# Performance work log

Hardware: AMD Instinct MI355X
Metric: run time of the kernel (lower is better)

## Reference

```python
import jax, jax.numpy as jnp
import numpy as np

DIM = 1024
NUM_HEADS = 16
HEAD_DIM = 64
SCALE = 1.0 / np.sqrt(float(HEAD_DIM))


def setup_inputs() -> dict:
    key = jax.random.key(0)
    ks = jax.random.split(key, 11)
    B, S, D = 2, 4096, DIM
    glorot = lambda k, shape: jax.random.uniform(
        k, shape, jnp.float32,
        -jnp.sqrt(6.0 / (shape[0] + shape[1])), jnp.sqrt(6.0 / (shape[0] + shape[1])))
    return {
        "x": jax.random.normal(ks[0], (B, S, D), jnp.float32),
        "Wq": glorot(ks[1], (D, NUM_HEADS * HEAD_DIM)),
        "bq": jnp.zeros((NUM_HEADS * HEAD_DIM,), jnp.float32),
        "Wk": glorot(ks[2], (D, NUM_HEADS * HEAD_DIM)),
        "bk": jnp.zeros((NUM_HEADS * HEAD_DIM,), jnp.float32),
        "Wv": glorot(ks[3], (D, NUM_HEADS * HEAD_DIM)),
        "bv": jnp.zeros((NUM_HEADS * HEAD_DIM,), jnp.float32),
        "Wqt": glorot(ks[4], (D, D)),
        "bqt": jnp.zeros((D,), jnp.float32),
        "Wo": glorot(ks[5], (D, D)),
        "bo": jnp.zeros((D,), jnp.float32),
        "num_anchor_tokens": 512,
    }


def _split_heads(t):
    # [B, T, H*Dh] -> [B, H, T, Dh]
    B, T, _ = t.shape
    return t.reshape(B, T, NUM_HEADS, HEAD_DIM).transpose(0, 2, 1, 3)


def reference(x, Wq, bq, Wk, bk, Wv, bv, Wqt, bqt, Wo, bo, num_anchor_tokens):
    B, S, D = x.shape
    A = num_anchor_tokens  # static Python int
    anchors = x[:, :A, :]            # [B, A, D]
    queries = x[:, A:, :]            # [B, S-A, D]

    anchor_q = _split_heads(anchors @ Wq + bq)   # [B, H, A, Dh]
    anchor_k = _split_heads(anchors @ Wk + bk)   # [B, H, A, Dh]
    anchor_v = _split_heads(anchors @ Wv + bv)   # [B, H, A, Dh]
    query_q = _split_heads(queries @ Wqt + bqt)  # [B, H, S-A, Dh]

    combined_q = jnp.concatenate([anchor_q, query_q], axis=2)  # [B, H, S, Dh]
    scores = jnp.einsum("bhsd,bhad->bhsa", combined_q, anchor_k) * SCALE
    attn = jax.nn.softmax(scores, axis=-1)        # [B, H, S, A]
    out = jnp.einsum("bhsa,bhad->bhsd", attn, anchor_v)  # [B, H, S, Dh]
    out = out.transpose(0, 2, 1, 3).reshape(B, S, D)
    return out @ Wo + bo
```

## Files before the change

### kernel.cpp

```cpp
#include <hip/hip_runtime.h>
#include <hip/hip_bf16.h>
#include <math.h>
#include <stdint.h>

typedef _Float16 f16;
typedef _Float16 f16x8 __attribute__((ext_vector_type(8)));
typedef _Float16 f16x4 __attribute__((ext_vector_type(4)));
typedef float f32x4 __attribute__((ext_vector_type(4)));

#define DIM   1024
#define NH    16
#define HD    64
#define BB    2
#define SS    4096
#define AA    512
#define SCALE 0.125f
#define EXP_C1 0.18033688011112043f
#define EXP_C2 (-2.8853900817779268f)

#define GLOAD_LDS16(g, l)                                                                   \
  __builtin_amdgcn_global_load_lds((const __attribute__((address_space(1))) uint32_t*)(g),  \
                                   (__attribute__((address_space(3))) uint32_t*)(l), 16, 0, 0)

static const size_t OFF_XH  = 0;
static const size_t OFF_WT  = 8388608;
static const size_t OFF_QC  = OFF_WT + 5u*1048576u;
static const size_t OFF_KB  = OFF_QC + 8388608u;
static const size_t OFF_VT  = OFF_KB + 1048576u;
static const size_t OFF_AO  = OFF_VT + 1048576u;

__global__ __launch_bounds__(256) void cast_x_kernel(const float* __restrict__ x,
                                                     f16* __restrict__ xh) {
    size_t i = ((size_t)blockIdx.x * 256 + threadIdx.x) * 4;
    float4 v = *reinterpret_cast<const float4*>(x + i);
    f16x4 o;
    o[0] = (f16)v.x; o[1] = (f16)v.y; o[2] = (f16)v.z; o[3] = (f16)v.w;
    *reinterpret_cast<f16x4*>(xh + i) = o;
}

__global__ __launch_bounds__(256) void wcast_kernel(const float* W0, const float* W1,
                                                    const float* W2, const float* W3,
                                                    const float* W4,
                                                    f16* T0, f16* T1, f16* T2, f16* T3, f16* T4) {
    __shared__ float tile[32][33];
    const float* W; f16* T;
    switch (blockIdx.z) {
        case 0: W = W0; T = T0; break;
        case 1: W = W1; T = T1; break;
        case 2: W = W2; T = T2; break;
        case 3: W = W3; T = T3; break;
        default: W = W4; T = T4; break;
    }
    int tx = threadIdx.x, ty = threadIdx.y;
    int gx = blockIdx.x * 32, gy = blockIdx.y * 32;
#pragma unroll
    for (int i = 0; i < 32; i += 8)
        tile[ty + i][tx] = W[(size_t)(gy + ty + i) * DIM + gx + tx];
    __syncthreads();
#pragma unroll
    for (int i = 0; i < 32; i += 8)
        T[(size_t)(gx + ty + i) * DIM + gy + tx] = (f16)tile[tx][ty + i];
}

struct GemmOut {
    const f16* Bt;
    const float* bias;
    int mode;
    void* out;
    int sdim;
    int soff;
};

__global__ __launch_bounds__(256) void gemm_kernel(const f16* __restrict__ A,
                                                   int rows_per_b, int a_row_off,
                                                   GemmOut o0, GemmOut o1, GemmOut o2) {
    __shared__ __align__(16) f16 As[128 * 32];
    __shared__ __align__(16) f16 Bs[128 * 32];

    GemmOut o = (blockIdx.z == 0) ? o0 : ((blockIdx.z == 1) ? o1 : o2);

    const int t    = threadIdx.x;
    const int wid  = t >> 6;
    const int lane = t & 63;
    const int lr   = lane & 15;
    const int lg   = lane >> 4;
    const int br   = blockIdx.x, bc = blockIdx.y;

    const int b      = (br * 128) / rows_per_b;
    const int s_base = (br * 128) % rows_per_b;

    const int srow = (wid << 4) + (lane >> 2);
    const int sch  = ((lane & 3) ^ ((lane >> 3) & 3)) << 3;
    const f16* Ap = A + ((size_t)b * SS + a_row_off + s_base + srow) * DIM + sch;
    const f16* Bp = o.Bt + ((size_t)(bc * 128 + srow)) * DIM + sch;
    f16* AsB = As + (wid << 9);
    f16* BsB = Bs + (wid << 9);

    const int wr = (wid >> 1) * 64;
    const int wc = (wid & 1) * 64;

    f32x4 acc[4][4] = {};

    for (int k0 = 0; k0 < DIM; k0 += 32) {
        GLOAD_LDS16(Ap + k0, AsB);
        GLOAD_LDS16(Ap + k0 + (size_t)64 * DIM, AsB + 2048);
        GLOAD_LDS16(Bp + k0, BsB);
        GLOAD_LDS16(Bp + k0 + (size_t)64 * DIM, BsB + 2048);
        __syncthreads();

        f16x8 af[4], bf[4];
#pragma unroll
        for (int m = 0; m < 4; m++) {
            const int r = wr + m * 16 + lr;
            af[m] = *reinterpret_cast<const f16x8*>(&As[r * 32 + ((lg ^ ((r >> 1) & 3)) << 3)]);
        }
#pragma unroll
        for (int n = 0; n < 4; n++) {
            const int r = wc + n * 16 + lr;
            bf[n] = *reinterpret_cast<const f16x8*>(&Bs[r * 32 + ((lg ^ ((r >> 1) & 3)) << 3)]);
        }
#pragma unroll
        for (int m = 0; m < 4; m++)
#pragma unroll
            for (int n = 0; n < 4; n++)
                acc[m][n] = __builtin_amdgcn_mfma_f32_16x16x32_f16(af[m], bf[n], acc[m][n], 0, 0, 0);
        __syncthreads();
    }

#pragma unroll
    for (int m = 0; m < 4; m++) {
        const int row_local = wr + m * 16 + lg * 4;
#pragma unroll
        for (int n = 0; n < 4; n++) {
            const int c  = bc * 128 + wc + n * 16 + lr;
            const float bv = o.bias[c];
            const int h = c >> 6, d = c & 63;
#pragma unroll
            for (int q = 0; q < 4; q++) {
                const int s_local = s_base + row_local + q;
                const float val = acc[m][n][q] + bv;
                if (o.mode == 2) {
                    ((float*)o.out)[((size_t)b * SS + o.soff + s_local) * DIM + c] = val;
                } else if (o.mode == 0) {
                    const int out_s = o.soff + s_local;
                    ((f16*)o.out)[(((size_t)(b * NH + h)) * o.sdim + out_s) * HD + d] = (f16)val;
                } else {
                    ((f16*)o.out)[(((size_t)(b * NH + h)) * HD + d) * AA + (o.soff + s_local)] = (f16)val;
                }
            }
        }
    }
}

__global__ __launch_bounds__(256) void attn_kernel(const f16* __restrict__ qc,
                                                   const f16* __restrict__ kb,
                                                   const f16* __restrict__ vt,
                                                   f16* __restrict__ ao) {
    __shared__ __align__(16) f16 Ks[2][64 * 64];
    __shared__ __align__(16) f16 Vs[2][64 * 64];
    __shared__ __align__(16) f16 Ps[4][16][64];

    const int t    = threadIdx.x;
    const int wid  = t >> 6;
    const int lane = t & 63;
    const int lr   = lane & 15;
    const int lg   = lane >> 4;
    const int qt   = blockIdx.x;
    const int h    = blockIdx.y;
    const int b    = blockIdx.z;
    const size_t bh = (size_t)b * NH + h;

    const int qrow = qt * 64 + wid * 16 + lr;
    const f16* qp = qc + (bh * SS + qrow) * HD + lg * 8;
    const f16x8 qa0 = *reinterpret_cast<const f16x8*>(qp);
    const f16x8 qa1 = *reinterpret_cast<const f16x8*>(qp + 32);

    const int sr_k = wid * 16 + (lane >> 3);
    const f16* kg = kb + bh * (size_t)AA * HD;
    const f16* vg = vt + bh * (size_t)HD * AA;

    f32x4 acc[4] = {};
    float rsum[4] = {0.f, 0.f, 0.f, 0.f};

#define ATTN_STAGE(buf, a0)                                                          \
    {                                                                                \
        _Pragma("unroll")                                                            \
        for (int i = 0; i < 2; i++) {                                                \
            const int r  = sr_k + i * 8;                                             \
            const int ck = (((lane & 7) ^ (r & 7)) << 3);                            \
            GLOAD_LDS16(kg + (size_t)((a0) + r) * HD + ck,                           \
                        &Ks[buf][(wid * 16 + i * 8) * 64]);                          \
            GLOAD_LDS16(vg + (size_t)r * AA + (a0) + ck,                             \
                        &Vs[buf][(wid * 16 + i * 8) * 64]);                          \
        }                                                                            \
    }

    ATTN_STAGE(0, 0);
    asm volatile("s_waitcnt vmcnt(0)");
    __syncthreads();

    int cur = 0;
    for (int at = 0; at < AA / 64; ++at) {
        if (at < AA / 64 - 1) ATTN_STAGE(cur ^ 1, (at + 1) * 64);

        f32x4 s[4];
#pragma unroll
        for (int n = 0; n < 4; n++) {
            const int r = n * 16 + lr;
            const int x = r & 7;
            f16x8 kf0 = *reinterpret_cast<const f16x8*>(&Ks[cur][r * 64 + ((lg ^ x) << 3)]);
            f16x8 kf1 = *reinterpret_cast<const f16x8*>(&Ks[cur][r * 64 + (((lg + 4) ^ x) << 3)]);
            f32x4 z = {};
            z = __builtin_amdgcn_mfma_f32_16x16x32_f16(qa0, kf0, z, 0, 0, 0);
            z = __builtin_amdgcn_mfma_f32_16x16x32_f16(qa1, kf1, z, 0, 0, 0);
            s[n] = z;
        }

#pragma unroll
        for (int n = 0; n < 4; n++) {
#pragma unroll
            for (int q = 0; q < 4; q++) {
                const float p = exp2f(fmaf(s[n][q], EXP_C1, EXP_C2));
                rsum[q] += p;
                const int row = lg * 4 + q;
                Ps[wid][row][(((2 * n + (lr >> 3)) ^ (row & 7)) << 3) + (lr & 7)] = (f16)p;
            }
        }
        const f16x8 pa0 = *reinterpret_cast<const f16x8*>(&Ps[wid][lr][(lg ^ (lr & 7)) << 3]);
        const f16x8 pa1 = *reinterpret_cast<const f16x8*>(&Ps[wid][lr][((lg + 4) ^ (lr & 7)) << 3]);

#pragma unroll
        for (int n = 0; n < 4; n++) {
            const int d = n * 16 + lr;
            const int x = d & 7;
            f16x8 vf0 = *reinterpret_cast<const f16x8*>(&Vs[cur][d * 64 + ((lg ^ x) << 3)]);
            f16x8 vf1 = *reinterpret_cast<const f16x8*>(&Vs[cur][d * 64 + (((lg + 4) ^ x) << 3)]);
            acc[n] = __builtin_amdgcn_mfma_f32_16x16x32_f16(pa0, vf0, acc[n], 0, 0, 0);
            acc[n] = __builtin_amdgcn_mfma_f32_16x16x32_f16(pa1, vf1, acc[n], 0, 0, 0);
        }

        asm volatile("s_waitcnt vmcnt(0)");
        __syncthreads();
        cur ^= 1;
    }

#pragma unroll
    for (int off = 1; off < 16; off <<= 1) {
#pragma unroll
        for (int q = 0; q < 4; q++) rsum[q] += __shfl_xor(rsum[q], off);
    }
#pragma unroll
    for (int q = 0; q < 4; q++) {
        const float inv = 1.0f / rsum[q];
        const int row = qt * 64 + wid * 16 + lg * 4 + q;
#pragma unroll
        for (int n = 0; n < 4; n++) {
            ao[((size_t)b * SS + row) * DIM + h * HD + n * 16 + lr] = (f16)(acc[n][q] * inv);
        }
    }
}

extern "C" void kernel_launch(void* const* d_in, const int* in_sizes, int n_in,
                              void* d_out, int out_size, void* d_ws, size_t ws_size,
                              hipStream_t stream) {
    const float* x   = (const float*)d_in[0];
    const float* Wq  = (const float*)d_in[1];
    const float* bq  = (const float*)d_in[2];
    const float* Wk  = (const float*)d_in[3];
    const float* bk  = (const float*)d_in[4];
    const float* Wv  = (const float*)d_in[5];
    const float* bv  = (const float*)d_in[6];
    const float* Wqt = (const float*)d_in[7];
    const float* bqt = (const float*)d_in[8];
    const float* Wo  = (const float*)d_in[9];
    const float* bo  = (const float*)d_in[10];

    f16* ws   = (f16*)d_ws;
    f16* xh   = ws + OFF_XH;
    f16* wtq  = ws + OFF_WT;
    f16* wtk  = wtq + 1048576u;
    f16* wtv  = wtk + 1048576u;
    f16* wtqt = wtv + 1048576u;
    f16* wto  = wtqt + 1048576u;
    f16* qc   = ws + OFF_QC;
    f16* kbuf = ws + OFF_KB;
    f16* vtb  = ws + OFF_VT;
    f16* ao   = ws + OFF_AO;

    cast_x_kernel<<<8192, 256, 0, stream>>>(x, xh);
    wcast_kernel<<<dim3(32, 32, 5), dim3(32, 8), 0, stream>>>(Wq, Wk, Wv, Wqt, Wo,
                                                              wtq, wtk, wtv, wtqt, wto);

    GemmOut oq { wtq, bq, 0, qc,   SS, 0 };
    GemmOut ok { wtk, bk, 0, kbuf, AA, 0 };
    GemmOut ov { wtv, bv, 1, vtb,  AA, 0 };
    gemm_kernel<<<dim3(8, 8, 3), 256, 0, stream>>>(xh, 512, 0, oq, ok, ov);

    GemmOut oqt { wtqt, bqt, 0, qc, SS, 512 };
    gemm_kernel<<<dim3(56, 8, 1), 256, 0, stream>>>(xh, 3584, 512, oqt, oqt, oqt);

    attn_kernel<<<dim3(64, NH, BB), 256, 0, stream>>>(qc, kbuf, vtb, ao);

    GemmOut oo { wto, bo, 2, d_out, SS, 0 };
    gemm_kernel<<<dim3(64, 8, 1), 256, 0, stream>>>(ao, 4096, 0, oo, oo, oo);
}
```

Measured before the change: 145.1 us.

## Double-buffer GEMM loads, merge projection launches, enlarge attention query tiles

The GEMM k-loop now double-buffers its LDS tiles, issuing the next global-to-LDS load before computing the current tile, to hide load latency. The two projection GEMM launches are merged into one kernel whose blocks branch by index to the Q, Q-tail, K or V weights, which removes one launch and lets the blocks run together. The attention kernel handles 128 query rows per block, two 16-row groups per wave, so each loaded K/V tile is reused twice and half as many blocks are launched. The explicit vmcnt waits are dropped in favour of __syncthreads alone, which is a correctness risk if the LDS-direct loads are not covered by the barrier.

```diff
diff --git a/kernel.cpp b/kernel.cpp
--- a/kernel.cpp
+++ b/kernel.cpp
@@ -62,22 +62,116 @@
         T[(size_t)(gx + ty + i) * DIM + gy + tx] = (f16)tile[tx][ty + i];
 }
 
-struct GemmOut {
-    const f16* Bt;
-    const float* bias;
-    int mode;
-    void* out;
-    int sdim;
-    int soff;
-};
-
-__global__ __launch_bounds__(256) void gemm_kernel(const f16* __restrict__ A,
-                                                   int rows_per_b, int a_row_off,
-                                                   GemmOut o0, GemmOut o1, GemmOut o2) {
-    __shared__ __align__(16) f16 As[128 * 32];
-    __shared__ __align__(16) f16 Bs[128 * 32];
-
-    GemmOut o = (blockIdx.z == 0) ? o0 : ((blockIdx.z == 1) ? o1 : o2);
+#define G_STAGE(buf, k0)                                               \
+    {                                                                  \
+        GLOAD_LDS16(Ap + (k0), &As[buf][wid << 9]);                    \
+        GLOAD_LDS16(Ap + (k0) + (size_t)64 * DIM,                      \
+                    &As[buf][(wid << 9) + 2048]);                      \
+        GLOAD_LDS16(Bp + (k0), &Bs[buf][wid << 9]);                    \
+        GLOAD_LDS16(Bp + (k0) + (size_t)64 * DIM,                      \
+                    &Bs[buf][(wid << 9) + 2048]);                      \
+    }
+
+#define G_KLOOP                                                                                   \
+    G_STAGE(0, 0);                                                                                \
+    __syncthreads();                                                                              \
+    int cur = 0;                                                                                  \
+    for (int k0 = 0; k0 < DIM; k0 += 32) {                                                        \
+        if (k0 + 32 < DIM) G_STAGE(cur ^ 1, k0 + 32);                                             \
+        f16x8 af[4], bf[4];                                                                       \
+        _Pragma("unroll")                                                                         \
+        for (int m = 0; m < 4; m++) {                                                             \
+            const int r = wr + m * 16 + lr;                                                       \
+            af[m] = *reinterpret_cast<const f16x8*>(&As[cur][r * 32 + ((lg ^ ((r >> 1) & 3)) << 3)]); \
+        }                                                                                         \
+        _Pragma("unroll")                                                                         \
+        for (int n = 0; n < 4; n++) {                                                             \
+            const int r = wc + n * 16 + lr;                                                       \
+            bf[n] = *reinterpret_cast<const f16x8*>(&Bs[cur][r * 32 + ((lg ^ ((r >> 1) & 3)) << 3)]); \
+        }                                                                                         \
+        _Pragma("unroll")                                                                         \
+        for (int m = 0; m < 4; m++)                                                               \
+            _Pragma("unroll")                                                                     \
+            for (int n = 0; n < 4; n++)                                                           \
+                acc[m][n] = __builtin_amdgcn_mfma_f32_16x16x32_f16(af[m], bf[n], acc[m][n], 0, 0, 0); \
+        __syncthreads();                                                                          \
+        cur ^= 1;                                                                                 \
+    }
+
+__global__ __launch_bounds__(256) void proj_kernel(const f16* __restrict__ xh,
+                                                   const f16* __restrict__ wtq,
+                                                   const f16* __restrict__ wtqt,
+                                                   const f16* __restrict__ wtk,
+                                                   const f16* __restrict__ wtv,
+                                                   const float* __restrict__ bq,
+                                                   const float* __restrict__ bqt,
+                                                   const float* __restrict__ bk,
+                                                   const float* __restrict__ bv,
+                                                   f16* __restrict__ qc,
+                                                   f16* __restrict__ kbuf,
+                                                   f16* __restrict__ vtb) {
+    __shared__ __align__(16) f16 As[2][4096];
+    __shared__ __align__(16) f16 Bs[2][4096];
+
+    const int t    = threadIdx.x;
+    const int wid  = t >> 6;
+    const int lane = t & 63;
+    const int lr   = lane & 15;
+    const int lg   = lane >> 4;
+    const int x    = blockIdx.x, bc = blockIdx.y;
+
+    int b, srow0, mode, sdim;
+    const f16* Bt; const float* bias; f16* outp;
+    if (x < 64) {
+        b = x >> 5; srow0 = (x & 31) * 128;
+        if (srow0 < 512) { Bt = wtq; bias = bq; } else { Bt = wtqt; bias = bqt; }
+        mode = 0; sdim = SS; outp = qc;
+    } else if (x < 72) {
+        int y = x - 64; b = y >> 2; srow0 = (y & 3) * 128;
+        Bt = wtk; bias = bk; mode = 0; sdim = AA; outp = kbuf;
+    } else {
+        int y = x - 72; b = y >> 2; srow0 = (y & 3) * 128;
+        Bt = wtv; bias = bv; mode = 1; sdim = AA; outp = vtb;
+    }
+
+    const int srow = (wid << 4) + (lane >> 2);
+    const int sch  = ((lane & 3) ^ ((lane >> 3) & 3)) << 3;
+    const f16* Ap = xh + ((size_t)b * SS + srow0 + srow) * DIM + sch;
+    const f16* Bp = Bt + ((size_t)(bc * 128 + srow)) * DIM + sch;
+
+    const int wr = (wid >> 1) * 64;
+    const int wc = (wid & 1) * 64;
+
+    f32x4 acc[4][4] = {};
+    G_KLOOP
+
+#pragma unroll
+    for (int m = 0; m < 4; m++) {
+        const int row_local = wr + m * 16 + lg * 4;
+#pragma unroll
+        for (int n = 0; n < 4; n++) {
+            const int c  = bc * 128 + wc + n * 16 + lr;
+            const float bvv = bias[c];
+            const int h = c >> 6, d = c & 63;
+#pragma unroll
+            for (int q = 0; q < 4; q++) {
+                const int s_g = srow0 + row_local + q;
+                const float val = acc[m][n][q] + bvv;
+                if (mode == 0)
+                    outp[(((size_t)(b * NH + h)) * sdim + s_g) * HD + d] = (f16)val;
+                else
+                    outp[(((size_t)(b * NH + h)) * HD + d) * AA + s_g] = (f16)val;
+            }
+        }
+    }
+}
+
+__global__ __launch_bounds__(256) void final_gemm(const f16* __restrict__ ao,
+                                                  const f16* __restrict__ wto,
+                                                  const float* __restrict__ bo,
+                                                  float* __restrict__ out) {
+    __shared__ __align__(16) f16 As[2][4096];
+    __shared__ __align__(16) f16 Bs[2][4096];
 
     const int t    = threadIdx.x;
     const int wid  = t >> 6;
@@ -86,46 +180,19 @@
     const int lg   = lane >> 4;
     const int br   = blockIdx.x, bc = blockIdx.y;
 
-    const int b      = (br * 128) / rows_per_b;
-    const int s_base = (br * 128) % rows_per_b;
+    const int b     = br >> 5;
+    const int srow0 = (br & 31) * 128;
 
     const int srow = (wid << 4) + (lane >> 2);
     const int sch  = ((lane & 3) ^ ((lane >> 3) & 3)) << 3;
-    const f16* Ap = A + ((size_t)b * SS + a_row_off + s_base + srow) * DIM + sch;
-    const f16* Bp = o.Bt + ((size_t)(bc * 128 + srow)) * DIM + sch;
-    f16* AsB = As + (wid << 9);
-    f16* BsB = Bs + (wid << 9);
+    const f16* Ap = ao + ((size_t)b * SS + srow0 + srow) * DIM + sch;
+    const f16* Bp = wto + ((size_t)(bc * 128 + srow)) * DIM + sch;
 
     const int wr = (wid >> 1) * 64;
     const int wc = (wid & 1) * 64;
 
     f32x4 acc[4][4] = {};
-
-    for (int k0 = 0; k0 < DIM; k0 += 32) {
-        GLOAD_LDS16(Ap + k0, AsB);
-        GLOAD_LDS16(Ap + k0 + (size_t)64 * DIM, AsB + 2048);
-        GLOAD_LDS16(Bp + k0, BsB);
-        GLOAD_LDS16(Bp + k0 + (size_t)64 * DIM, BsB + 2048);
-        __syncthreads();
-
-        f16x8 af[4], bf[4];
-#pragma unroll
-        for (int m = 0; m < 4; m++) {
-            const int r = wr + m * 16 + lr;
-            af[m] = *reinterpret_cast<const f16x8*>(&As[r * 32 + ((lg ^ ((r >> 1) & 3)) << 3)]);
-        }
-#pragma unroll
-        for (int n = 0; n < 4; n++) {
-            const int r = wc + n * 16 + lr;
-            bf[n] = *reinterpret_cast<const f16x8*>(&Bs[r * 32 + ((lg ^ ((r >> 1) & 3)) << 3)]);
-        }
-#pragma unroll
-        for (int m = 0; m < 4; m++)
-#pragma unroll
-            for (int n = 0; n < 4; n++)
-                acc[m][n] = __builtin_amdgcn_mfma_f32_16x16x32_f16(af[m], bf[n], acc[m][n], 0, 0, 0);
-        __syncthreads();
-    }
+    G_KLOOP
 
 #pragma unroll
     for (int m = 0; m < 4; m++) {
@@ -133,21 +200,10 @@
 #pragma unroll
         for (int n = 0; n < 4; n++) {
             const int c  = bc * 128 + wc + n * 16 + lr;
-            const float bv = o.bias[c];
-            const int h = c >> 6, d = c & 63;
-#pragma unroll
-            for (int q = 0; q < 4; q++) {
-                const int s_local = s_base + row_local + q;
-                const float val = acc[m][n][q] + bv;
-                if (o.mode == 2) {
-                    ((float*)o.out)[((size_t)b * SS + o.soff + s_local) * DIM + c] = val;
-                } else if (o.mode == 0) {
-                    const int out_s = o.soff + s_local;
-                    ((f16*)o.out)[(((size_t)(b * NH + h)) * o.sdim + out_s) * HD + d] = (f16)val;
-                } else {
-                    ((f16*)o.out)[(((size_t)(b * NH + h)) * HD + d) * AA + (o.soff + s_local)] = (f16)val;
-                }
-            }
+            const float bvv = bo[c];
+#pragma unroll
+            for (int q = 0; q < 4; q++)
+                out[((size_t)b * SS + srow0 + row_local + q) * DIM + c] = acc[m][n][q] + bvv;
         }
     }
 }
@@ -170,17 +226,21 @@
     const int b    = blockIdx.z;
     const size_t bh = (size_t)b * NH + h;
 
-    const int qrow = qt * 64 + wid * 16 + lr;
-    const f16* qp = qc + (bh * SS + qrow) * HD + lg * 8;
-    const f16x8 qa0 = *reinterpret_cast<const f16x8*>(qp);
-    const f16x8 qa1 = *reinterpret_cast<const f16x8*>(qp + 32);
+    f16x8 qa[2][2];
+#pragma unroll
+    for (int g = 0; g < 2; g++) {
+        const int qrow = qt * 128 + wid * 32 + g * 16 + lr;
+        const f16* qp = qc + (bh * SS + qrow) * HD + lg * 8;
+        qa[g][0] = *reinterpret_cast<const f16x8*>(qp);
+        qa[g][1] = *reinterpret_cast<const f16x8*>(qp + 32);
+    }
 
     const int sr_k = wid * 16 + (lane >> 3);
     const f16* kg = kb + bh * (size_t)AA * HD;
     const f16* vg = vt + bh * (size_t)HD * AA;
 
-    f32x4 acc[4] = {};
-    float rsum[4] = {0.f, 0.f, 0.f, 0.f};
+    f32x4 acc[2][4] = {};
+    float rsum[2][4] = {};
 
 #define ATTN_STAGE(buf, a0)                                                          \
     {                                                                                \
@@ -196,68 +256,74 @@
     }
 
     ATTN_STAGE(0, 0);
-    asm volatile("s_waitcnt vmcnt(0)");
     __syncthreads();
 
     int cur = 0;
     for (int at = 0; at < AA / 64; ++at) {
         if (at < AA / 64 - 1) ATTN_STAGE(cur ^ 1, (at + 1) * 64);
 
-        f32x4 s[4];
+        f32x4 s[2][4];
 #pragma unroll
         for (int n = 0; n < 4; n++) {
             const int r = n * 16 + lr;
-            const int x = r & 7;
-            f16x8 kf0 = *reinterpret_cast<const f16x8*>(&Ks[cur][r * 64 + ((lg ^ x) << 3)]);
-            f16x8 kf1 = *reinterpret_cast<const f16x8*>(&Ks[cur][r * 64 + (((lg + 4) ^ x) << 3)]);
-            f32x4 z = {};
-            z = __builtin_amdgcn_mfma_f32_16x16x32_f16(qa0, kf0, z, 0, 0, 0);
-            z = __builtin_amdgcn_mfma_f32_16x16x32_f16(qa1, kf1, z, 0, 0, 0);
-            s[n] = z;
-        }
-
-#pragma unroll
-        for (int n = 0; n < 4; n++) {
-#pragma unroll
-            for (int q = 0; q < 4; q++) {
-                const float p = exp2f(fmaf(s[n][q], EXP_C1, EXP_C2));
-                rsum[q] += p;
-                const int row = lg * 4 + q;
-                Ps[wid][row][(((2 * n + (lr >> 3)) ^ (row & 7)) << 3) + (lr & 7)] = (f16)p;
+            const int xk = r & 7;
+            f16x8 kf0 = *reinterpret_cast<const f16x8*>(&Ks[cur][r * 64 + ((lg ^ xk) << 3)]);
+            f16x8 kf1 = *reinterpret_cast<const f16x8*>(&Ks[cur][r * 64 + (((lg + 4) ^ xk) << 3)]);
+#pragma unroll
+            for (int g = 0; g < 2; g++) {
+                f32x4 z = {};
+                z = __builtin_amdgcn_mfma_f32_16x16x32_f16(qa[g][0], kf0, z, 0, 0, 0);
+                z = __builtin_amdgcn_mfma_f32_16x16x32_f16(qa[g][1], kf1, z, 0, 0, 0);
+                s[g][n] = z;
             }
         }
-        const f16x8 pa0 = *reinterpret_cast<const f16x8*>(&Ps[wid][lr][(lg ^ (lr & 7)) << 3]);
-        const f16x8 pa1 = *reinterpret_cast<const f16x8*>(&Ps[wid][lr][((lg + 4) ^ (lr & 7)) << 3]);
-
-#pragma unroll
-        for (int n = 0; n < 4; n++) {
-            const int d = n * 16 + lr;
-            const int x = d & 7;
-            f16x8 vf0 = *reinterpret_cast<const f16x8*>(&Vs[cur][d * 64 + ((lg ^ x) << 3)]);
-            f16x8 vf1 = *reinterpret_cast<const f16x8*>(&Vs[cur][d * 64 + (((lg + 4) ^ x) << 3)]);
-            acc[n] = __builtin_amdgcn_mfma_f32_16x16x32_f16(pa0, vf0, acc[n], 0, 0, 0);
-            acc[n] = __builtin_amdgcn_mfma_f32_16x16x32_f16(pa1, vf1, acc[n], 0, 0, 0);
-        }
-
-        asm volatile("s_waitcnt vmcnt(0)");
+
+#pragma unroll
+        for (int g = 0; g < 2; g++) {
+#pragma unroll
+            for (int n = 0; n < 4; n++) {
+#pragma unroll
+                for (int q = 0; q < 4; q++) {
+                    const float p = exp2f(fmaf(s[g][n][q], EXP_C1, EXP_C2));
+                    rsum[g][q] += p;
+                    const int row = lg * 4 + q;
+                    Ps[wid][row][(((2 * n + (lr >> 3)) ^ (row & 7)) << 3) + (lr & 7)] = (f16)p;
+                }
+            }
+            const f16x8 pa0 = *reinterpret_cast<const f16x8*>(&Ps[wid][lr][(lg ^ (lr & 7)) << 3]);
+            const f16x8 pa1 = *reinterpret_cast<const f16x8*>(&Ps[wid][lr][((lg + 4) ^ (lr & 7)) << 3]);
+#pragma unroll
+            for (int n = 0; n < 4; n++) {
+                const int d = n * 16 + lr;
+                const int xv = d & 7;
+                f16x8 vf0 = *reinterpret_cast<const f16x8*>(&Vs[cur][d * 64 + ((lg ^ xv) << 3)]);
+                f16x8 vf1 = *reinterpret_cast<const f16x8*>(&Vs[cur][d * 64 + (((lg + 4) ^ xv) << 3)]);
+                acc[g][n] = __builtin_amdgcn_mfma_f32_16x16x32_f16(pa0, vf0, acc[g][n], 0, 0, 0);
+                acc[g][n] = __builtin_amdgcn_mfma_f32_16x16x32_f16(pa1, vf1, acc[g][n], 0, 0, 0);
+            }
+        }
+
         __syncthreads();
         cur ^= 1;
     }
 
 #pragma unroll
-    for (int off = 1; off < 16; off <<= 1) {
-#pragma unroll
-        for (int q = 0; q < 4; q++) rsum[q] += __shfl_xor(rsum[q], off);
-    }
-#pragma unroll
-    for (int q = 0; q < 4; q++) {
-        const float inv = 1.0f / rsum[q];
-        const int row = qt * 64 + wid * 16 + lg * 4 + q;
-#pragma unroll
-        for (int n = 0; n < 4; n++) {
-            ao[((size_t)b * SS + row) * DIM + h * HD + n * 16 + lr] = (f16)(acc[n][q] * inv);
-        }
-    }
+    for (int off = 1; off < 16; off <<= 1)
+#pragma unroll
+        for (int g = 0; g < 2; g++)
+#pragma unroll
+            for (int q = 0; q < 4; q++) rsum[g][q] += __shfl_xor(rsum[g][q], off);
+
+#pragma unroll
+    for (int g = 0; g < 2; g++)
+#pragma unroll
+        for (int q = 0; q < 4; q++) {
+            const float inv = 1.0f / rsum[g][q];
+            const int row = qt * 128 + wid * 32 + g * 16 + lg * 4 + q;
+#pragma unroll
+            for (int n = 0; n < 4; n++)
+                ao[((size_t)b * SS + row) * DIM + h * HD + n * 16 + lr] = (f16)(acc[g][n][q] * inv);
+        }
 }
 
 extern "C" void kernel_launch(void* const* d_in, const int* in_sizes, int n_in,
@@ -291,16 +357,10 @@
     wcast_kernel<<<dim3(32, 32, 5), dim3(32, 8), 0, stream>>>(Wq, Wk, Wv, Wqt, Wo,
                                                               wtq, wtk, wtv, wtqt, wto);
 
-    GemmOut oq { wtq, bq, 0, qc,   SS, 0 };
-    GemmOut ok { wtk, bk, 0, kbuf, AA, 0 };
-    GemmOut ov { wtv, bv, 1, vtb,  AA, 0 };
-    gemm_kernel<<<dim3(8, 8, 3), 256, 0, stream>>>(xh, 512, 0, oq, ok, ov);
-
-    GemmOut oqt { wtqt, bqt, 0, qc, SS, 512 };
-    gemm_kernel<<<dim3(56, 8, 1), 256, 0, stream>>>(xh, 3584, 512, oqt, oqt, oqt);
-
-    attn_kernel<<<dim3(64, NH, BB), 256, 0, stream>>>(qc, kbuf, vtb, ao);
-
-    GemmOut oo { wto, bo, 2, d_out, SS, 0 };
-    gemm_kernel<<<dim3(64, 8, 1), 256, 0, stream>>>(ao, 4096, 0, oo, oo, oo);
-}
+    proj_kernel<<<dim3(80, 8), 256, 0, stream>>>(xh, wtq, wtqt, wtk, wtv,
+                                                 bq, bqt, bk, bv, qc, kbuf, vtb);
+
+    attn_kernel<<<dim3(32, NH, BB), 256, 0, stream>>>(qc, kbuf, vtb, ao);
+
+    final_gemm<<<dim3(64, 8), 256, 0, stream>>>(ao, wto, bo, (float*)d_out);
+}
```

Result: faster. 127.5 us (-12.1%).
